# Optimization experiments

Hardware: AMD Instinct MI355X
Metric: run time of the kernel (lower is better)

The kernel has to match this reference:

```python
import jax, jax.numpy as jnp
import numpy as np

NUM_CLASSES = 81
TOP_K = 200
CONF_THRESH = 0.01
NMS_THRESH = 0.45
VAR0, VAR1 = 0.1, 0.2  # SSD Config['variance']


def decode(loc, priors):
    # loc: [..., P, 4], priors: [P, 4] (cx, cy, w, h)
    cxcy = priors[:, :2] + loc[..., :2] * VAR0 * priors[:, 2:]
    wh = priors[:, 2:] * jnp.exp(loc[..., 2:] * VAR1)
    x1y1 = cxcy - wh * 0.5
    x2y2 = x1y1 + wh
    return jnp.concatenate([x1y1, x2y2], axis=-1)  # [..., P, 4] xyxy


def nms_class(boxes, scores):
    # boxes: [P, 4], scores: [P] -> [TOP_K, 5] rows of (score, x1, y1, x2, y2)
    K = TOP_K
    masked = jnp.where(scores > CONF_THRESH, scores, -jnp.inf)
    top_scores, idx = jax.lax.top_k(masked, K)          # descending
    cand = boxes[idx]                                   # [K, 4]
    valid = jnp.isfinite(top_scores)
    x1, y1, x2, y2 = cand[:, 0], cand[:, 1], cand[:, 2], cand[:, 3]
    area = (x2 - x1) * (y2 - y1)
    iw = jnp.maximum(jnp.minimum(x2[:, None], x2[None, :]) - jnp.maximum(x1[:, None], x1[None, :]), 0.0)
    ih = jnp.maximum(jnp.minimum(y2[:, None], y2[None, :]) - jnp.maximum(y1[:, None], y1[None, :]), 0.0)
    inter = iw * ih
    union = area[:, None] + area[None, :] - inter
    iou = jnp.where(union > 0, inter / jnp.where(union > 0, union, 1.0), 0.0)  # [K, K]
    ar = jnp.arange(K)

    def step(suppressed, i):
        kept = valid[i] & ~suppressed[i]
        suppressed = suppressed | (kept & (iou[i] > NMS_THRESH) & (ar > i))
        return suppressed, kept

    _, keep = jax.lax.scan(step, jnp.zeros(K, dtype=bool), ar)  # [K] bool
    rows = jnp.concatenate([jnp.where(valid, top_scores, 0.0)[:, None], cand], axis=1)  # [K, 5]
    # compact kept rows to the front (score-descending order), zeros after
    tgt = jnp.where(keep, jnp.cumsum(keep) - 1, K)
    out = jnp.zeros((K + 1, 5), rows.dtype).at[tgt].set(rows)[:K]
    return out


def detect(loc_data, conf_data, prior_data):
    boxes = decode(loc_data, prior_data)                 # [B, P, 4]
    conf = jnp.transpose(conf_data, (0, 2, 1))           # [B, C, P]
    per_image = jax.vmap(nms_class, in_axes=(None, 0))   # over classes
    out = jax.vmap(per_image, in_axes=(0, 0))(boxes, conf)  # [B, C, K, 5]
    out = out.at[:, 0].set(0.0)  # background class skipped (cl starts at 1)
    return out


def setup_inputs() -> dict:
    key = jax.random.key(0)
    k1, k2, k3 = jax.random.split(key, 3)
    B, P, C = 32, 24564, NUM_CLASSES
    loc_data = jax.random.normal(k1, (B, P, 4), dtype=jnp.float32)
    conf_data = jax.random.uniform(k2, (B, P, C), dtype=jnp.float32)
    prior_data = jax.random.uniform(k3, (P, 4), dtype=jnp.float32)
    return {"loc_data": loc_data, "conf_data": conf_data, "prior_data": prior_data}


def reference(loc_data, conf_data, prior_data):
    return detect(loc_data, conf_data, prior_data)
```

## Files before the change

kernel.cpp:

```cpp
#include <hip/hip_runtime.h>
#include <hip/hip_bf16.h>
#include <math.h>

constexpr int B_ = 32;
constexpr int P_ = 24564;
constexpr int C_ = 81;
constexpr int K_ = 200;

constexpr int NCH = 64;
constexpr int CPR = 384;
constexpr int SCAP = 1024;
constexpr int CAP  = 512;
constexpr float T_SEL = 0.9869f;

__global__ __launch_bounds__(256) void k_filter(const float* __restrict__ conf,
                                                unsigned long long* __restrict__ cand,
                                                unsigned* __restrict__ cnt,
                                                unsigned* __restrict__ bflag) {
    __shared__ unsigned long long skey[SCAP];
    __shared__ unsigned short scls[SCAP];
    __shared__ unsigned scnt[C_], sbase[C_], scnt2[C_];
    __shared__ unsigned sn;
    const int bid = blockIdx.x;
    const int b = bid / NCH, ch = bid % NCH;
    const int tid = threadIdx.x;

    for (int i = tid; i < C_; i += 256) { scnt[i] = 0; scnt2[i] = 0; }
    if (tid == 0) sn = 0;
    __syncthreads();

    const int p0 = ch * CPR;
    const int rows = min(CPR, P_ - p0);
    const float* slab = conf + ((size_t)b * P_ + (size_t)p0) * C_;
    const int n4 = rows * C_ / 4;
    for (int g = tid; g < n4; g += 256) {
        float4 v = ((const float4*)slab)[g];
        int e = g * 4;
        int c = e % C_;
        int pl = e / C_;
        float s[4] = {v.x, v.y, v.z, v.w};
#pragma unroll
        for (int j = 0; j < 4; ++j) {
            int cj = c + j, pj = pl;
            if (cj >= C_) { cj -= C_; pj += 1; }
            float sv = s[j];
            if (sv > T_SEL && cj != 0) {
                unsigned pos = atomicAdd(&sn, 1u);
                if (pos < (unsigned)SCAP) {
                    unsigned pg = (unsigned)(p0 + pj);
                    skey[pos] = ((unsigned long long)__float_as_uint(sv) << 32) | (~pg);
                    scls[pos] = (unsigned short)cj;
                    atomicAdd(&scnt[cj], 1u);
                } else {
                    bflag[b] = 1u;
                }
            }
        }
    }
    __syncthreads();
    if (tid < C_) sbase[tid] = scnt[tid] ? atomicAdd(&cnt[b * C_ + tid], scnt[tid]) : 0u;
    __syncthreads();
    const int m = (int)min(sn, (unsigned)SCAP);
    for (int i = tid; i < m; i += 256) {
        int c = scls[i];
        unsigned pos = sbase[c] + atomicAdd(&scnt2[c], 1u);
        if (pos < (unsigned)CAP)
            cand[((size_t)(b * C_ + c)) * CAP + pos] = skey[i];
    }
}

__global__ __launch_bounds__(256) void k_nms(const unsigned long long* __restrict__ cand,
                                             const unsigned* __restrict__ cnt,
                                             const unsigned* __restrict__ bflag,
                                             const float* __restrict__ conf,
                                             const float* __restrict__ loc,
                                             const float* __restrict__ prior,
                                             float* __restrict__ out) {
#pragma clang fp contract(off)
    __shared__ __align__(16) unsigned long long masks[K_][4];
    __shared__ __align__(16) float outrow[1024];
    __shared__ unsigned long long top[256];
    __shared__ float sc[K_], bx1[K_], by1[K_], bx2[K_], by2[K_], bar[K_];
    __shared__ unsigned char vflag[K_];
    __shared__ unsigned long long keepw[4];
    __shared__ unsigned kpre[4];
    __shared__ unsigned long long sh_prefix;
    __shared__ unsigned sh_rank, sh_cnt2;

    unsigned long long* buf = (unsigned long long*)outrow;
    unsigned* rs_hist = (unsigned*)&masks[0][0];
    unsigned* rs_sf   = rs_hist + 256;

    const int bid = blockIdx.x;
    const int b = bid / C_, c = bid % C_;
    const int tid = threadIdx.x;
    float* obase = out + ((size_t)(b * C_ + c)) * (K_ * 5);

    if (c == 0) {
        float4 z = make_float4(0.f, 0.f, 0.f, 0.f);
        for (int i = tid; i < K_ * 5 / 4; i += 256) ((float4*)obase)[i] = z;
        return;
    }

    const int task = b * C_ + c;
    const unsigned long long* crow = cand + (size_t)task * CAP;
    const unsigned cn = cnt[task];
    const bool fb = (bflag[b] != 0u) || (cn < (unsigned)K_) || (cn > (unsigned)CAP);

    int n;
    if (!fb) {
        n = (int)cn;
        for (int i = tid; i < CAP; i += 256)
            buf[i] = (i < n) ? crow[i] : 0ull;
        top[tid] = 0ull;
        __syncthreads();
    } else {
        for (int i = tid; i < CAP; i += 256) buf[i] = 0ull;
        top[tid] = 0ull;
        const float* col = conf + (size_t)b * P_ * C_ + c;
        unsigned lc = 0;
        for (int p = tid; p < P_; p += 256)
            if (col[(size_t)p * C_] > 0.01f) lc++;
        rs_sf[tid] = lc;
        __syncthreads();
        for (int off = 128; off > 0; off >>= 1) {
            if (tid < off) rs_sf[tid] += rs_sf[tid + off];
            __syncthreads();
        }
        const unsigned total = rs_sf[0];
        unsigned long long t200v = 1ull;
        if (total > (unsigned)K_) {
            if (tid == 0) { sh_prefix = 0ull; sh_rank = (unsigned)K_; }
            __syncthreads();
            for (int d = 7; d >= 0; --d) {
                rs_hist[tid] = 0;
                __syncthreads();
                const unsigned long long pref = sh_prefix;
                const unsigned rank = sh_rank;
                for (int p = tid; p < P_; p += 256) {
                    float sv = col[(size_t)p * C_];
                    if (sv > 0.01f) {
                        unsigned long long key =
                            ((unsigned long long)__float_as_uint(sv) << 32) | (~(unsigned)p);
                        bool match = (d == 7) || (((key ^ pref) >> ((d + 1) * 8)) == 0ull);
                        if (match) atomicAdd(&rs_hist[(unsigned)((key >> (d * 8)) & 255ull)], 1u);
                    }
                }
                __syncthreads();
                rs_sf[tid] = rs_hist[tid];
                __syncthreads();
                for (int off = 1; off < 256; off <<= 1) {
                    unsigned v2 = (tid + off < 256) ? rs_sf[tid + off] : 0u;
                    __syncthreads();
                    rs_sf[tid] += v2;
                    __syncthreads();
                }
                if (rs_sf[tid] >= rank && (tid == 255 || rs_sf[tid + 1] < rank)) {
                    sh_prefix = pref | ((unsigned long long)tid << (d * 8));
                    sh_rank = rank - ((tid == 255) ? 0u : rs_sf[tid + 1]);
                }
                __syncthreads();
            }
            t200v = sh_prefix;
        }
        if (tid == 0) sh_cnt2 = 0;
        __syncthreads();
        for (int p = tid; p < P_; p += 256) {
            float sv = col[(size_t)p * C_];
            if (sv > 0.01f) {
                unsigned long long key =
                    ((unsigned long long)__float_as_uint(sv) << 32) | (~(unsigned)p);
                if (key >= t200v) {
                    unsigned pos = atomicAdd(&sh_cnt2, 1u);
                    if (pos < (unsigned)CAP) buf[pos] = key;
                }
            }
        }
        __syncthreads();
        n = (int)min(sh_cnt2, (unsigned)CAP);
    }

    {
        const unsigned long long k1 = buf[tid];
        const unsigned long long k2 = buf[tid + 256];
        int r1 = 0, r2 = 0;
        const int nn = (n + 3) & ~3;
        for (int i = 0; i < nn; i += 4) {
            ulonglong2 a = *(const ulonglong2*)&buf[i];
            ulonglong2 bb = *(const ulonglong2*)&buf[i + 2];
            r1 += (a.x > k1) + (a.y > k1) + (bb.x > k1) + (bb.y > k1);
            r2 += (a.x > k2) + (a.y > k2) + (bb.x > k2) + (bb.y > k2);
        }
        if (k1 != 0ull && r1 < 256) top[r1] = k1;
        if (k2 != 0ull && r2 < 256) top[r2] = k2;
    }
    __syncthreads();

    const int nsel = min(n, K_);

    if (tid < K_) {
        const int r = tid;
        bool v = (r < nsel);
        float score = 0.f, x1 = 0.f, y1 = 0.f, x2 = 0.f, y2 = 0.f, ar = 0.f;
        if (v) {
            unsigned long long key = top[r];
            unsigned ub = (unsigned)(key >> 32);
            unsigned p = ~((unsigned)key);
            score = __uint_as_float(ub);
            v = ((ub & 0x7F800000u) != 0x7F800000u);
            const float4 l4 = ((const float4*)loc)[(size_t)b * P_ + p];
            const float4 p4 = ((const float4*)prior)[p];
            float cx = p4.x + (l4.x * 0.1f) * p4.z;
            float cy = p4.y + (l4.y * 0.1f) * p4.w;
            float w  = p4.z * expf(l4.z * 0.2f);
            float h  = p4.w * expf(l4.w * 0.2f);
            x1 = cx - w * 0.5f;
            y1 = cy - h * 0.5f;
            x2 = x1 + w;
            y2 = y1 + h;
            ar = (x2 - x1) * (y2 - y1);
        }
        sc[r] = score; bx1[r] = x1; by1[r] = y1; bx2[r] = x2; by2[r] = y2; bar[r] = ar;
        vflag[r] = v ? (unsigned char)1 : (unsigned char)0;
    }
    __syncthreads();

    for (int i = tid; i < 1024; i += 256) outrow[i] = 0.0f;

    const int nv = nsel;
    const int wid = tid >> 6, lane = tid & 63;

    float jx1[4], jy1[4], jx2[4], jy2[4], jar[4];
#pragma unroll
    for (int w = 0; w < 4; ++w) {
        int j = w * 64 + lane;
        bool in = (j < K_);
        jx1[w] = in ? bx1[j] : 0.f;
        jy1[w] = in ? by1[j] : 0.f;
        jx2[w] = in ? bx2[j] : 0.f;
        jy2[w] = in ? by2[j] : 0.f;
        jar[w] = in ? bar[j] : 0.f;
    }

    for (int idx = tid; idx < K_ * 4; idx += 256) {
        int i = idx >> 2, w = idx & 3;
        if (w < (i >> 6)) masks[i][w] = 0ull;
    }
    for (int i = wid; i < nv; i += 4) {
        float r_x1 = bx1[i], r_y1 = by1[i], r_x2 = bx2[i], r_y2 = by2[i], r_ar = bar[i];
        const int w0 = i >> 6;
#pragma unroll
        for (int w = 0; w < 4; ++w) {
            if (w >= w0) {
                int j = w * 64 + lane;
                bool pred = false;
                if (j < nv && j > i) {
                    float xx1 = fmaxf(r_x1, jx1[w]);
                    float yy1 = fmaxf(r_y1, jy1[w]);
                    float xx2 = fminf(r_x2, jx2[w]);
                    float yy2 = fminf(r_y2, jy2[w]);
                    float iw = fmaxf(xx2 - xx1, 0.0f);
                    float ih = fmaxf(yy2 - yy1, 0.0f);
                    float inter = iw * ih;
                    float uni = (r_ar + jar[w]) - inter;
                    pred = (uni > 0.0f) && (inter / uni > 0.45f);
                }
                unsigned long long m = __ballot(pred);
                if (lane == 0) masks[i][w] = m;
            }
        }
    }
    __syncthreads();

    if (tid < 64) {
        const int l = tid;
        unsigned long long V0 = __ballot((l       < nv) && vflag[l]);
        unsigned long long V1 = __ballot((64 + l  < nv) && vflag[64 + l]);
        unsigned long long V2 = __ballot((128 + l < nv) && vflag[128 + l]);
        unsigned long long V3 = __ballot((192 + l < nv) && vflag[192 + l]);
        auto rownz = [&](int r) -> bool {
            if (r >= nv) return false;
            return (masks[r][0] | masks[r][1] | masks[r][2] | masks[r][3]) != 0ull;
        };
        unsigned long long R0 = __ballot(rownz(l))       & V0;
        unsigned long long R1 = __ballot(rownz(64 + l))  & V1;
        unsigned long long R2 = __ballot(rownz(128 + l)) & V2;
        unsigned long long R3 = __ballot(rownz(192 + l)) & V3;

        unsigned long long S0 = 0, S1 = 0, S2 = 0, S3 = 0;
        while (true) {
            unsigned long long t;
            int i = -1;
            if ((t = R0 & ~S0) != 0ull)      i = (int)__builtin_ctzll(t);
            else if ((t = R1 & ~S1) != 0ull) i = 64 + (int)__builtin_ctzll(t);
            else if ((t = R2 & ~S2) != 0ull) i = 128 + (int)__builtin_ctzll(t);
            else if ((t = R3 & ~S3) != 0ull) i = 192 + (int)__builtin_ctzll(t);
            if (i < 0) break;
            const unsigned long long bit = 1ull << (i & 63);
            const int slot = i >> 6;
            if (slot == 0) R0 ^= bit; else if (slot == 1) R1 ^= bit;
            else if (slot == 2) R2 ^= bit; else R3 ^= bit;
            ulonglong2 m01 = *(const ulonglong2*)&masks[i][0];
            ulonglong2 m23 = *(const ulonglong2*)&masks[i][2];
            S0 |= m01.x; S1 |= m01.y; S2 |= m23.x; S3 |= m23.y;
        }
        if (l == 0) {
            unsigned long long K0 = V0 & ~S0, K1 = V1 & ~S1, K2 = V2 & ~S2, K3 = V3 & ~S3;
            keepw[0] = K0; keepw[1] = K1; keepw[2] = K2; keepw[3] = K3;
            kpre[0] = 0;
            kpre[1] = (unsigned)__popcll(K0);
            kpre[2] = kpre[1] + (unsigned)__popcll(K1);
            kpre[3] = kpre[2] + (unsigned)__popcll(K2);
        }
    }
    __syncthreads();

    if (tid < nv) {
        int w = tid >> 6, bit = tid & 63;
        if ((keepw[w] >> bit) & 1ull) {
            unsigned slot = kpre[w] + (unsigned)__popcll(keepw[w] & ((1ull << bit) - 1ull));
            outrow[slot * 5 + 0] = sc[tid];
            outrow[slot * 5 + 1] = bx1[tid];
            outrow[slot * 5 + 2] = by1[tid];
            outrow[slot * 5 + 3] = bx2[tid];
            outrow[slot * 5 + 4] = by2[tid];
        }
    }
    __syncthreads();

    for (int i = tid; i < K_ * 5 / 4; i += 256)
        ((float4*)obase)[i] = ((const float4*)outrow)[i];
}

extern "C" void kernel_launch(void* const* d_in, const int* in_sizes, int n_in,
                              void* d_out, int out_size, void* d_ws, size_t ws_size,
                              hipStream_t stream) {
    const float* loc   = (const float*)d_in[0];
    const float* conf  = (const float*)d_in[1];
    const float* prior = (const float*)d_in[2];
    float* out = (float*)d_out;

    char* ws = (char*)d_ws;
    const size_t candBytes = (size_t)B_ * C_ * CAP * sizeof(unsigned long long);
    unsigned long long* cand = (unsigned long long*)ws;
    unsigned* cnt   = (unsigned*)(ws + candBytes);
    unsigned* bflag = cnt + (size_t)B_ * C_;

    hipMemsetAsync(cnt, 0, (size_t)(B_ * C_ + B_) * sizeof(unsigned), stream);

    k_filter<<<B_ * NCH, 256, 0, stream>>>(conf, cand, cnt, bflag);
    k_nms   <<<B_ * C_,  256, 0, stream>>>(cand, cnt, bflag, conf, loc, prior, out);
}
```

Before: 167.1 us.

## Prefilter candidates with score histogram before rank sort; pack boxes as float4

Measured after the change: 156.7 us. -6.2%, faster.

```diff
diff --git a/kernel.cpp b/kernel.cpp
--- a/kernel.cpp
+++ b/kernel.cpp
@@ -79,17 +79,19 @@
 #pragma clang fp contract(off)
     __shared__ __align__(16) unsigned long long masks[K_][4];
     __shared__ __align__(16) float outrow[1024];
-    __shared__ unsigned long long top[256];
-    __shared__ float sc[K_], bx1[K_], by1[K_], bx2[K_], by2[K_], bar[K_];
+    __shared__ __align__(16) unsigned long long top[256];
+    __shared__ __align__(16) float4 bbox[K_];
+    __shared__ float sc[K_], bar[K_];
     __shared__ unsigned char vflag[K_];
     __shared__ unsigned long long keepw[4];
     __shared__ unsigned kpre[4];
     __shared__ unsigned long long sh_prefix;
-    __shared__ unsigned sh_rank, sh_cnt2;
+    __shared__ unsigned sh_rank, sh_cnt2, sh_cut, sh_fat;
 
     unsigned long long* buf = (unsigned long long*)outrow;
     unsigned* rs_hist = (unsigned*)&masks[0][0];
-    unsigned* rs_sf   = rs_hist + 256;
+    unsigned* rs_sf   = (unsigned*)&masks[32][0];
+    unsigned long long* srt = &masks[64][0];
 
     const int bid = blockIdx.x;
     const int b = bid / C_, c = bid % C_;
@@ -113,6 +115,7 @@
         for (int i = tid; i < CAP; i += 256)
             buf[i] = (i < n) ? crow[i] : 0ull;
         top[tid] = 0ull;
+        rs_hist[tid] = 0u;
         __syncthreads();
     } else {
         for (int i = tid; i < CAP; i += 256) buf[i] = 0ull;
@@ -180,19 +183,74 @@
         n = (int)min(sh_cnt2, (unsigned)CAP);
     }
 
-    {
+    bool fat = false;
+    if (n <= 256) {
+        top[tid] = (tid < n) ? buf[tid] : 0ull;
+        __syncthreads();
+    } else {
+        for (int i = tid; i < n; i += 256)
+            atomicAdd(&rs_hist[(unsigned)((buf[i] >> 43) & 255ull)], 1u);
+        __syncthreads();
+        if (tid < 64) {
+            const int l = tid;
+            uint4 h = *(const uint4*)&rs_hist[l * 4];
+            unsigned s3 = h.w;
+            unsigned s2 = h.z + s3;
+            unsigned s1 = h.y + s2;
+            unsigned s0 = h.x + s1;
+            unsigned acc = s0;
+            for (int off = 1; off < 64; off <<= 1) {
+                unsigned o = __shfl_down(acc, off, 64);
+                if (l + off < 64) acc += o;
+            }
+            const unsigned suf_after = acc - s0;
+            unsigned long long bal = __ballot(s0 + suf_after >= (unsigned)K_);
+            int hl = 63 - __builtin_clzll(bal);
+            if (l == hl) {
+                int k; unsigned sufk;
+                if      (s3 + suf_after >= (unsigned)K_) { k = 3; sufk = s3 + suf_after; }
+                else if (s2 + suf_after >= (unsigned)K_) { k = 2; sufk = s2 + suf_after; }
+                else if (s1 + suf_after >= (unsigned)K_) { k = 1; sufk = s1 + suf_after; }
+                else                                     { k = 0; sufk = s0 + suf_after; }
+                sh_cut = (unsigned)(l * 4 + k);
+                sh_fat = (sufk > 256u) ? 1u : 0u;
+                sh_cnt2 = 0u;
+            }
+        }
+        __syncthreads();
+        fat = (sh_fat != 0u);
+        if (!fat) {
+            const unsigned cut = sh_cut;
+            for (int i = tid; i < n; i += 256) {
+                unsigned long long key = buf[i];
+                if ((unsigned)((key >> 43) & 255ull) >= cut)
+                    top[atomicAdd(&sh_cnt2, 1u)] = key;
+            }
+            __syncthreads();
+        }
+    }
+
+    if (!fat) {
+        const unsigned long long k1 = top[tid];
+        int r1 = 0;
+        for (int i = 0; i < 256; i += 4) {
+            ulonglong2 a  = *(const ulonglong2*)&top[i];
+            ulonglong2 b2 = *(const ulonglong2*)&top[i + 2];
+            r1 += (a.x > k1) + (a.y > k1) + (b2.x > k1) + (b2.y > k1);
+        }
+        if (k1 != 0ull) srt[r1] = k1;
+    } else {
         const unsigned long long k1 = buf[tid];
         const unsigned long long k2 = buf[tid + 256];
         int r1 = 0, r2 = 0;
-        const int nn = (n + 3) & ~3;
-        for (int i = 0; i < nn; i += 4) {
-            ulonglong2 a = *(const ulonglong2*)&buf[i];
-            ulonglong2 bb = *(const ulonglong2*)&buf[i + 2];
-            r1 += (a.x > k1) + (a.y > k1) + (bb.x > k1) + (bb.y > k1);
-            r2 += (a.x > k2) + (a.y > k2) + (bb.x > k2) + (bb.y > k2);
-        }
-        if (k1 != 0ull && r1 < 256) top[r1] = k1;
-        if (k2 != 0ull && r2 < 256) top[r2] = k2;
+        for (int i = 0; i < 512; i += 4) {
+            ulonglong2 a  = *(const ulonglong2*)&buf[i];
+            ulonglong2 b2 = *(const ulonglong2*)&buf[i + 2];
+            r1 += (a.x > k1) + (a.y > k1) + (b2.x > k1) + (b2.y > k1);
+            r2 += (a.x > k2) + (a.y > k2) + (b2.x > k2) + (b2.y > k2);
+        }
+        if (k1 != 0ull && r1 < 256) srt[r1] = k1;
+        if (k2 != 0ull && r2 < 256) srt[r2] = k2;
     }
     __syncthreads();
 
@@ -203,7 +261,7 @@
         bool v = (r < nsel);
         float score = 0.f, x1 = 0.f, y1 = 0.f, x2 = 0.f, y2 = 0.f, ar = 0.f;
         if (v) {
-            unsigned long long key = top[r];
+            unsigned long long key = srt[r];
             unsigned ub = (unsigned)(key >> 32);
             unsigned p = ~((unsigned)key);
             score = __uint_as_float(ub);
@@ -220,25 +278,26 @@
             y2 = y1 + h;
             ar = (x2 - x1) * (y2 - y1);
         }
-        sc[r] = score; bx1[r] = x1; by1[r] = y1; bx2[r] = x2; by2[r] = y2; bar[r] = ar;
+        bbox[r] = make_float4(x1, y1, x2, y2);
+        sc[r] = score; bar[r] = ar;
         vflag[r] = v ? (unsigned char)1 : (unsigned char)0;
     }
     __syncthreads();
 
-    for (int i = tid; i < 1024; i += 256) outrow[i] = 0.0f;
+    {
+        float4 z = make_float4(0.f, 0.f, 0.f, 0.f);
+        ((float4*)outrow)[tid] = z;
+    }
 
     const int nv = nsel;
     const int wid = tid >> 6, lane = tid & 63;
 
-    float jx1[4], jy1[4], jx2[4], jy2[4], jar[4];
+    float4 jb[4]; float jar[4];
 #pragma unroll
     for (int w = 0; w < 4; ++w) {
         int j = w * 64 + lane;
         bool in = (j < K_);
-        jx1[w] = in ? bx1[j] : 0.f;
-        jy1[w] = in ? by1[j] : 0.f;
-        jx2[w] = in ? bx2[j] : 0.f;
-        jy2[w] = in ? by2[j] : 0.f;
+        jb[w]  = in ? bbox[j] : make_float4(0.f, 0.f, 0.f, 0.f);
         jar[w] = in ? bar[j] : 0.f;
     }
 
@@ -247,7 +306,8 @@
         if (w < (i >> 6)) masks[i][w] = 0ull;
     }
     for (int i = wid; i < nv; i += 4) {
-        float r_x1 = bx1[i], r_y1 = by1[i], r_x2 = bx2[i], r_y2 = by2[i], r_ar = bar[i];
+        float4 rb = bbox[i];
+        float r_ar = bar[i];
         const int w0 = i >> 6;
 #pragma unroll
         for (int w = 0; w < 4; ++w) {
@@ -255,10 +315,10 @@
                 int j = w * 64 + lane;
                 bool pred = false;
                 if (j < nv && j > i) {
-                    float xx1 = fmaxf(r_x1, jx1[w]);
-                    float yy1 = fmaxf(r_y1, jy1[w]);
-                    float xx2 = fminf(r_x2, jx2[w]);
-                    float yy2 = fminf(r_y2, jy2[w]);
+                    float xx1 = fmaxf(rb.x, jb[w].x);
+                    float yy1 = fmaxf(rb.y, jb[w].y);
+                    float xx2 = fminf(rb.z, jb[w].z);
+                    float yy2 = fminf(rb.w, jb[w].w);
                     float iw = fmaxf(xx2 - xx1, 0.0f);
                     float ih = fmaxf(yy2 - yy1, 0.0f);
                     float inter = iw * ih;
@@ -319,11 +379,12 @@
         int w = tid >> 6, bit = tid & 63;
         if ((keepw[w] >> bit) & 1ull) {
             unsigned slot = kpre[w] + (unsigned)__popcll(keepw[w] & ((1ull << bit) - 1ull));
+            float4 bb = bbox[tid];
             outrow[slot * 5 + 0] = sc[tid];
-            outrow[slot * 5 + 1] = bx1[tid];
-            outrow[slot * 5 + 2] = by1[tid];
-            outrow[slot * 5 + 3] = bx2[tid];
-            outrow[slot * 5 + 4] = by2[tid];
+            outrow[slot * 5 + 1] = bb.x;
+            outrow[slot * 5 + 2] = bb.y;
+            outrow[slot * 5 + 3] = bb.z;
+            outrow[slot * 5 + 4] = bb.w;
         }
     }
     __syncthreads();
```

## Rank candidates directly from global memory and write NMS output without LDS staging

Applied to the files above, without the earlier changes.

Result: no change. 167.4 us (+0.2%).

```diff
diff --git a/kernel.cpp b/kernel.cpp
--- a/kernel.cpp
+++ b/kernel.cpp
@@ -78,18 +78,18 @@
                                              float* __restrict__ out) {
 #pragma clang fp contract(off)
     __shared__ __align__(16) unsigned long long masks[K_][4];
-    __shared__ __align__(16) float outrow[1024];
-    __shared__ unsigned long long top[256];
-    __shared__ float sc[K_], bx1[K_], by1[K_], bx2[K_], by2[K_], bar[K_];
+    __shared__ __align__(16) float4 bbox[K_];
+    __shared__ float sc[K_], bar[K_];
     __shared__ unsigned char vflag[K_];
     __shared__ unsigned long long keepw[4];
     __shared__ unsigned kpre[4];
     __shared__ unsigned long long sh_prefix;
     __shared__ unsigned sh_rank, sh_cnt2;
 
-    unsigned long long* buf = (unsigned long long*)outrow;
-    unsigned* rs_hist = (unsigned*)&masks[0][0];
-    unsigned* rs_sf   = rs_hist + 256;
+    unsigned long long* buf = &masks[0][0];
+    unsigned* rs_hist = (unsigned*)&masks[128][0];
+    unsigned* rs_sf   = (unsigned*)&masks[160][0];
+    unsigned long long* srt = &masks[128][0];
 
     const int bid = blockIdx.x;
     const int b = bid / C_, c = bid % C_;
@@ -110,13 +110,27 @@
     int n;
     if (!fb) {
         n = (int)cn;
-        for (int i = tid; i < CAP; i += 256)
-            buf[i] = (i < n) ? crow[i] : 0ull;
-        top[tid] = 0ull;
+
+        const unsigned long long k1 = (tid < n)       ? crow[tid]       : 0ull;
+        const unsigned long long k2 = (tid + 256 < n) ? crow[tid + 256] : 0ull;
+        int r1 = 0, r2 = 0;
+        int i = 0;
+        for (; i + 4 <= n; i += 4) {
+            unsigned long long a0 = crow[i], a1 = crow[i + 1];
+            unsigned long long a2 = crow[i + 2], a3 = crow[i + 3];
+            r1 += (a0 > k1) + (a1 > k1) + (a2 > k1) + (a3 > k1);
+            r2 += (a0 > k2) + (a1 > k2) + (a2 > k2) + (a3 > k2);
+        }
+        for (; i < n; ++i) {
+            unsigned long long a = crow[i];
+            r1 += (a > k1);
+            r2 += (a > k2);
+        }
+        if (tid < n && r1 < K_)       srt[r1] = k1;
+        if (tid + 256 < n && r2 < K_) srt[r2] = k2;
         __syncthreads();
     } else {
         for (int i = tid; i < CAP; i += 256) buf[i] = 0ull;
-        top[tid] = 0ull;
         const float* col = conf + (size_t)b * P_ * C_ + c;
         unsigned lc = 0;
         for (int p = tid; p < P_; p += 256)
@@ -178,23 +192,14 @@
         }
         __syncthreads();
         n = (int)min(sh_cnt2, (unsigned)CAP);
-    }
-
-    {
-        const unsigned long long k1 = buf[tid];
-        const unsigned long long k2 = buf[tid + 256];
-        int r1 = 0, r2 = 0;
-        const int nn = (n + 3) & ~3;
-        for (int i = 0; i < nn; i += 4) {
-            ulonglong2 a = *(const ulonglong2*)&buf[i];
-            ulonglong2 bb = *(const ulonglong2*)&buf[i + 2];
-            r1 += (a.x > k1) + (a.y > k1) + (bb.x > k1) + (bb.y > k1);
-            r2 += (a.x > k2) + (a.y > k2) + (bb.x > k2) + (bb.y > k2);
-        }
-        if (k1 != 0ull && r1 < 256) top[r1] = k1;
-        if (k2 != 0ull && r2 < 256) top[r2] = k2;
-    }
-    __syncthreads();
+
+        const unsigned long long k1 = (tid < n) ? buf[tid] : 0ull;
+        int r1 = 0;
+        for (int i = 0; i < n; ++i) r1 += (buf[i] > k1);
+        __syncthreads();
+        if (tid < n && r1 < K_) srt[r1] = k1;
+        __syncthreads();
+    }
 
     const int nsel = min(n, K_);
 
@@ -203,7 +208,7 @@
         bool v = (r < nsel);
         float score = 0.f, x1 = 0.f, y1 = 0.f, x2 = 0.f, y2 = 0.f, ar = 0.f;
         if (v) {
-            unsigned long long key = top[r];
+            unsigned long long key = srt[r];
             unsigned ub = (unsigned)(key >> 32);
             unsigned p = ~((unsigned)key);
             score = __uint_as_float(ub);
@@ -220,25 +225,21 @@
             y2 = y1 + h;
             ar = (x2 - x1) * (y2 - y1);
         }
-        sc[r] = score; bx1[r] = x1; by1[r] = y1; bx2[r] = x2; by2[r] = y2; bar[r] = ar;
+        bbox[r] = make_float4(x1, y1, x2, y2);
+        sc[r] = score; bar[r] = ar;
         vflag[r] = v ? (unsigned char)1 : (unsigned char)0;
     }
     __syncthreads();
-
-    for (int i = tid; i < 1024; i += 256) outrow[i] = 0.0f;
 
     const int nv = nsel;
     const int wid = tid >> 6, lane = tid & 63;
 
-    float jx1[4], jy1[4], jx2[4], jy2[4], jar[4];
+    float4 jb[4]; float jar[4];
 #pragma unroll
     for (int w = 0; w < 4; ++w) {
         int j = w * 64 + lane;
         bool in = (j < K_);
-        jx1[w] = in ? bx1[j] : 0.f;
-        jy1[w] = in ? by1[j] : 0.f;
-        jx2[w] = in ? bx2[j] : 0.f;
-        jy2[w] = in ? by2[j] : 0.f;
+        jb[w]  = in ? bbox[j] : make_float4(0.f, 0.f, 0.f, 0.f);
         jar[w] = in ? bar[j] : 0.f;
     }
 
@@ -247,7 +248,8 @@
         if (w < (i >> 6)) masks[i][w] = 0ull;
     }
     for (int i = wid; i < nv; i += 4) {
-        float r_x1 = bx1[i], r_y1 = by1[i], r_x2 = bx2[i], r_y2 = by2[i], r_ar = bar[i];
+        float4 rb = bbox[i];
+        float r_ar = bar[i];
         const int w0 = i >> 6;
 #pragma unroll
         for (int w = 0; w < 4; ++w) {
@@ -255,10 +257,10 @@
                 int j = w * 64 + lane;
                 bool pred = false;
                 if (j < nv && j > i) {
-                    float xx1 = fmaxf(r_x1, jx1[w]);
-                    float yy1 = fmaxf(r_y1, jy1[w]);
-                    float xx2 = fminf(r_x2, jx2[w]);
-                    float yy2 = fminf(r_y2, jy2[w]);
+                    float xx1 = fmaxf(rb.x, jb[w].x);
+                    float yy1 = fmaxf(rb.y, jb[w].y);
+                    float xx2 = fminf(rb.z, jb[w].z);
+                    float yy2 = fminf(rb.w, jb[w].w);
                     float iw = fmaxf(xx2 - xx1, 0.0f);
                     float ih = fmaxf(yy2 - yy1, 0.0f);
                     float inter = iw * ih;
@@ -319,17 +321,17 @@
         int w = tid >> 6, bit = tid & 63;
         if ((keepw[w] >> bit) & 1ull) {
             unsigned slot = kpre[w] + (unsigned)__popcll(keepw[w] & ((1ull << bit) - 1ull));
-            outrow[slot * 5 + 0] = sc[tid];
-            outrow[slot * 5 + 1] = bx1[tid];
-            outrow[slot * 5 + 2] = by1[tid];
-            outrow[slot * 5 + 3] = bx2[tid];
-            outrow[slot * 5 + 4] = by2[tid];
-        }
-    }
-    __syncthreads();
-
-    for (int i = tid; i < K_ * 5 / 4; i += 256)
-        ((float4*)obase)[i] = ((const float4*)outrow)[i];
+            float4 bb = bbox[tid];
+            float* o = obase + slot * 5;
+            o[0] = sc[tid]; o[1] = bb.x; o[2] = bb.y; o[3] = bb.z; o[4] = bb.w;
+        }
+    }
+    {
+        const unsigned keptTotal = kpre[3] + (unsigned)__popcll(keepw[3]);
+        const int zbase = (int)keptTotal * 5;
+        const int ztot = K_ * 5 - zbase;
+        for (int e = tid; e < ztot; e += 256) obase[zbase + e] = 0.0f;
+    }
 }
 
 extern "C" void kernel_launch(void* const* d_in, const int* in_sizes, int n_in,
```
